# Kernel tuning notes

Measured on AMD Instinct MI355X. Metric: run time of the kernel, lower is better.

## Reference

```python
import jax, jax.numpy as jnp
import numpy as np

B, C, N = 8, 256, 1024
D, DK, DV, H, NB = 256, 16, 32, 8, 4
P = N + 1


def layernorm(x, g, b, eps=1e-5):
    m = x.mean(-1, keepdims=True)
    v = x.var(-1, keepdims=True)
    return (x - m) / jnp.sqrt(v + eps) * g + b


def bn_inf(x, g, b, mean, var, eps=1e-5):
    # x: [B, C', N]; stats over channel dim
    scale = (g / jnp.sqrt(var + eps))[None, :, None]
    shift = (b - mean * g / jnp.sqrt(var + eps))[None, :, None]
    return x * scale + shift


def softmax_with_policy(attn, policy, eps=1e-6):
    # attn: [B,H,P,P], policy: [B,P,1]
    n = attn.shape[-1]
    ap = policy.reshape(policy.shape[0], 1, 1, n)
    eye = jnp.eye(n, dtype=ap.dtype)[None, None]
    ap = ap + (1.0 - ap) * eye
    m = attn.max(-1, keepdims=True)
    e = jnp.exp(attn - m) * ap
    return (e + eps / n) / (e.sum(-1, keepdims=True) + eps)


def setup_inputs() -> dict:
    key = jax.random.key(0)
    ks = jax.random.split(key, 24)
    s = 0.02
    inp = {
        'x': jax.random.normal(ks[0], (B, C, N), jnp.float32),
        'policy': jnp.ones((B, P, 1), jnp.float32),
        'conv1_w': jax.random.normal(ks[1], (D, C), jnp.float32) * s,
        'conv2_w': jax.random.normal(ks[2], (D, D), jnp.float32) * s,
        'bn1_g': jnp.ones((D,), jnp.float32),
        'bn1_b': jnp.zeros((D,), jnp.float32),
        'bn1_m': jax.random.normal(ks[3], (D,), jnp.float32) * s,
        'bn1_v': jax.random.uniform(ks[4], (D,), jnp.float32, 0.5, 1.5),
        'bn2_g': jnp.ones((D,), jnp.float32),
        'bn2_b': jnp.zeros((D,), jnp.float32),
        'bn2_m': jax.random.normal(ks[5], (D,), jnp.float32) * s,
        'bn2_v': jax.random.uniform(ks[6], (D,), jnp.float32, 0.5, 1.5),
        'cls_token': jax.random.normal(ks[7], (D,), jnp.float32),
        'ln1_g': jnp.ones((NB, D), jnp.float32),
        'ln1_b': jnp.zeros((NB, D), jnp.float32),
        'ln2_g': jnp.ones((NB, D), jnp.float32),
        'ln2_b': jnp.zeros((NB, D), jnp.float32),
        'wq': jax.random.normal(ks[8], (NB, H * DK, D), jnp.float32) * np.sqrt(2.0 / (D + DK)).astype(np.float32),
        'wk': jax.random.normal(ks[9], (NB, H * DK, D), jnp.float32) * np.sqrt(2.0 / (D + DK)).astype(np.float32),
        'wv': jax.random.normal(ks[10], (NB, H * DV, D), jnp.float32) * np.sqrt(2.0 / (D + DV)).astype(np.float32),
        'fc_w': jax.random.normal(ks[11], (NB, D, H * DV), jnp.float32) * s,
        'ff_w1': jax.random.normal(ks[12], (NB, 2 * D, D), jnp.float32) * s,
        'ff_b1': jnp.zeros((NB, 2 * D), jnp.float32),
        'ff_w2': jax.random.normal(ks[13], (NB, D, 2 * D), jnp.float32) * s,
        'ff_b2': jnp.zeros((NB, D), jnp.float32),
    }
    return inp


def reference(x, policy, conv1_w, conv2_w, bn1_g, bn1_b, bn1_m, bn1_v,
              bn2_g, bn2_b, bn2_m, bn2_v, cls_token,
              ln1_g, ln1_b, ln2_g, ln2_b, wq, wk, wv, fc_w,
              ff_w1, ff_b1, ff_w2, ff_b2):
    # stem: 1x1 conv + BN(inference) + ReLU, twice. x: [B, C, N]
    h = jax.nn.relu(bn_inf(jnp.einsum('dc,bcn->bdn', conv1_w, x), bn1_g, bn1_b, bn1_m, bn1_v))
    h = jax.nn.relu(bn_inf(jnp.einsum('dc,bcn->bdn', conv2_w, h), bn2_g, bn2_b, bn2_m, bn2_v))
    h = h.transpose(0, 2, 1)  # [B, N, D]
    cls = jnp.broadcast_to(cls_token[None, None, :], (B, 1, D))
    h = jnp.concatenate([cls, h], axis=1)  # [B, P, D]

    scale = 1.0 / np.sqrt(DK).astype(np.float32)
    for i in range(NB):
        # attention
        y = layernorm(h, ln1_g[i], ln1_b[i])
        q = jnp.einsum('bnd,ed->bne', y, wq[i]).reshape(B, P, H, DK).transpose(0, 2, 1, 3)
        k = jnp.einsum('bnd,ed->bne', y, wk[i]).reshape(B, P, H, DK).transpose(0, 2, 1, 3)
        v = jnp.einsum('bnd,ed->bne', y, wv[i]).reshape(B, P, H, DV).transpose(0, 2, 1, 3)
        attn = jnp.einsum('bhlk,bhtk->bhlt', q, k) * scale
        attn = softmax_with_policy(attn, policy)
        o = jnp.einsum('bhlt,bhtv->bhlv', attn, v)  # [B,H,P,DV]
        o = o.transpose(0, 2, 1, 3).reshape(B, P, H * DV)
        h = h + jnp.einsum('bne,de->bnd', o, fc_w[i])
        # feed-forward
        y = layernorm(h, ln2_g[i], ln2_b[i])
        y = jax.nn.gelu(jnp.einsum('bnd,ed->bne', y, ff_w1[i]) + ff_b1[i], approximate=False)
        h = h + jnp.einsum('bne,de->bnd', y, ff_w2[i]) + ff_b2[i]
    return h
```

## Files before the change

kernel.cpp:

```cpp
#include <hip/hip_runtime.h>
#include <stdint.h>


typedef unsigned short u16;
typedef unsigned int   u32;
typedef __bf16 bf16x8 __attribute__((ext_vector_type(8)));
typedef float  f32x4  __attribute__((ext_vector_type(4)));
typedef float  f32x16 __attribute__((ext_vector_type(16)));
typedef u32    u32x4  __attribute__((ext_vector_type(4)));

#define DEV static __device__ __forceinline__

DEV float b2f(u16 h){ u32 u = ((u32)h) << 16; return __builtin_bit_cast(float, u); }
DEV u16 f2b(float f){ u32 u = __builtin_bit_cast(u32, f); u32 r = (u + 0x7fffu + ((u >> 16) & 1u)) >> 16; return (u16)r; }
DEV float gelu_f(float x){ return 0.5f * x * (1.0f + erff(x * 0.7071067811865475f)); }
DEV u32 cvtpk(float lo, float hi){
  u32 w;
  asm("v_cvt_pk_bf16_f32 %0, %1, %2" : "=v"(w) : "v"(lo), "v"(hi));
  return w;
}
DEV float exp2_(float x){ float r; asm("v_exp_f32 %0, %1" : "=v"(r) : "v"(x)); return r; }

typedef void __attribute__((address_space(1)))* gas_t;
typedef void __attribute__((address_space(3)))* las_t;
DEV void cp16(const void* g, void* l){
  __builtin_amdgcn_global_load_lds((gas_t)(uintptr_t)g, (las_t)(uintptr_t)l, 16, 0, 0);
}

struct Seg { const float* src; u16* dst; int n; int period; int dstride; int block0; float scale; };
struct SegPack { Seg s[8]; };

__global__ __launch_bounds__(256) void k_convert(SegPack p){
  int bid = blockIdx.x;
  int si = 0;
  #pragma unroll
  for (int i = 1; i < 8; i++) if (bid >= p.s[i].block0) si = i;
  const Seg sg = p.s[si];
  int e0 = (bid - sg.block0) * 2048 + threadIdx.x * 8;
  #pragma unroll
  for (int k = 0; k < 8; k++){
    int e = e0 + k;
    if (e < sg.n) sg.dst[(e / sg.period) * sg.dstride + (e % sg.period)] = f2b(sg.src[e] * sg.scale);
  }
}

__global__ __launch_bounds__(256) void k_transpose_x(const float* __restrict__ x, u16* __restrict__ xT){
  __shared__ float t[32][33];
  int b = blockIdx.z, ct = blockIdx.y, nt = blockIdx.x;
  int tx = threadIdx.x & 31, ty = threadIdx.x >> 5;
  const float* xp = x + ((size_t)b * 256 + ct * 32) * 1024 + nt * 32;
  #pragma unroll
  for (int k = 0; k < 4; k++) t[ty + 8*k][tx] = xp[(size_t)(ty + 8*k) * 1024 + tx];
  __syncthreads();
  u16* op = xT + ((size_t)b * 1024 + nt * 32) * 256 + ct * 32;
  #pragma unroll
  for (int k = 0; k < 4; k++) op[(size_t)(ty + 8*k) * 256 + tx] = f2b(t[tx][ty + 8*k]);
}

__global__ void k_cls(const float* __restrict__ cls, float* __restrict__ h){
  int d = threadIdx.x;
  #pragma unroll
  for (int b = 0; b < 8; b++) h[(size_t)b * 1025 * 256 + d] = cls[d];
}

__global__ __launch_bounds__(256) void k_ln(const float* __restrict__ h, const float* __restrict__ g,
                                            const float* __restrict__ bt, u16* __restrict__ y){
  int lane = threadIdx.x & 63, wv = threadIdx.x >> 6;
  long t = (long)blockIdx.x * 4 + wv;
  if (t >= 8200) return;
  const float* row = h + t * 256;
  float4 v = *reinterpret_cast<const float4*>(row + lane * 4);
  float s = v.x + v.y + v.z + v.w;
  float q = v.x*v.x + v.y*v.y + v.z*v.z + v.w*v.w;
  #pragma unroll
  for (int o = 32; o > 0; o >>= 1){ s += __shfl_xor(s, o); q += __shfl_xor(q, o); }
  float mean = s * (1.f/256.f);
  float var  = q * (1.f/256.f) - mean * mean;
  float rs = rsqrtf(var + 1e-5f);
  ushort4 ov;
  const float* vp = &v.x;
  u16* o16 = (u16*)&ov;
  #pragma unroll
  for (int j = 0; j < 4; j++){
    int c = lane * 4 + j;
    o16[j] = f2b((vp[j] - mean) * rs * g[c] + bt[c]);
  }
  *reinterpret_cast<ushort4*>(y + t * 256 + lane * 4) = ov;
}

template<int EPI, int BM, int BN>
__global__ __launch_bounds__(256) void k_gemmT(const u16* __restrict__ A, const u16* __restrict__ W,
    int M, int K, int E, float* __restrict__ outF, u16* __restrict__ outB,
    u16* __restrict__ outK,
    const float* __restrict__ a0, const float* __restrict__ a1,
    const float* __restrict__ a2, const float* __restrict__ a3){
  constexpr int MR = BM / 32, NR = BN / 32;
  __shared__ __align__(16) u16 As[BM * 64];
  __shared__ __align__(16) u16 Bs[BN * 64];
  const int tid = threadIdx.x;
  const int lane = tid & 63, wv = tid >> 6;
  const int wr = wv >> 1, wc = wv & 1;
  const int tM = blockIdx.x * BM, tN = blockIdx.y * BN;
  f32x4 acc[MR][NR];
  #pragma unroll
  for (int m = 0; m < MR; m++)
    #pragma unroll
    for (int n = 0; n < NR; n++)
      #pragma unroll
      for (int j = 0; j < 4; j++) acc[m][n][j] = 0.f;

  const int l8 = lane >> 3, lm = lane & 7;
  for (int k0 = 0; k0 < K; k0 += 64){
    __syncthreads();
    #pragma unroll
    for (int is = 0; is < BM / 32; is++){
      int row = is * 32 + wv * 8 + l8;
      int kg = lm ^ (row & 7);
      int ra = tM + row; ra = ra < M ? ra : M - 1;
      cp16(A + (size_t)ra * K + k0 + kg * 8, As + is * 2048 + wv * 512);
    }
    #pragma unroll
    for (int is = 0; is < BN / 32; is++){
      int row = is * 32 + wv * 8 + l8;
      int kg = lm ^ (row & 7);
      cp16(W + (size_t)(tN + row) * K + k0 + kg * 8, Bs + is * 2048 + wv * 512);
    }
    __syncthreads();
    #pragma unroll
    for (int kk = 0; kk < 2; kk++){
      bf16x8 af[MR], bfv[NR];
      #pragma unroll
      for (int m = 0; m < MR; m++){
        int row = wr * (BM/2) + m * 16 + (lane & 15);
        int kg = (kk * 4 + (lane >> 4)) ^ (row & 7);
        af[m] = *reinterpret_cast<const bf16x8*>(&As[row * 64 + kg * 8]);
      }
      #pragma unroll
      for (int n = 0; n < NR; n++){
        int row = wc * (BN/2) + n * 16 + (lane & 15);
        int kg = (kk * 4 + (lane >> 4)) ^ (row & 7);
        bfv[n] = *reinterpret_cast<const bf16x8*>(&Bs[row * 64 + kg * 8]);
      }
      #pragma unroll
      for (int m = 0; m < MR; m++)
        #pragma unroll
        for (int n = 0; n < NR; n++)
          acc[m][n] = __builtin_amdgcn_mfma_f32_16x16x32_bf16(af[m], bfv[n], acc[m][n], 0, 0, 0);
    }
  }
  #pragma unroll
  for (int n = 0; n < NR; n++){
    const int col = tN + wc * (BN/2) + n * 16 + (lane & 15);
    float scale = 0.f, shift = 0.f, bias = 0.f;
    if (EPI == 1 || EPI == 2){
      float gv = a0[col], bv = a1[col], mv = a2[col], vv = a3[col];
      scale = gv * rsqrtf(vv + 1e-5f);
      shift = bv - mv * scale;
    }
    if (EPI == 4 || EPI == 5) bias = a0[col];
    #pragma unroll
    for (int m = 0; m < MR; m++){
      const int row0 = tM + wr * (BM/2) + m * 16 + ((lane >> 4) << 2);
      #pragma unroll
      for (int j = 0; j < 4; j++){
        int r = row0 + j;
        if (r < M){
          float v = acc[m][n][j];
          if (EPI == 1){ v = v * scale + shift; v = v > 0.f ? v : 0.f; outB[(size_t)r * E + col] = f2b(v); }
          else if (EPI == 2){ v = v * scale + shift; v = v > 0.f ? v : 0.f; outF[(size_t)(r + (r >> 10) + 1) * 256 + col] = v; }
          else if (EPI == 3){ outF[(size_t)r * E + col] += v; }
          else if (EPI == 4){ outB[(size_t)r * E + col] = f2b(gelu_f(v + bias)); }
          else if (EPI == 5){ outF[(size_t)r * E + col] += v + bias; }
          else {
            int bb = r / 1025, tok = r - bb * 1025;
            if (col < 128){
              outB[(size_t)r * 512 + col] = f2b(v);
            } else if (col < 256){
              int hk = (col - 128) >> 4, dk = col & 15;
              outK[((size_t)((bb * 8 + hk) * 1032 + tok)) * 16 + dk] = f2b(v);
            } else {
              u16 bv = f2b(v);
              outB[(size_t)r * 512 + col] = bv;
              u16* vt = (u16*)outF;
              int hv = (col - 256) >> 5, dv = (col - 256) & 31;
              vt[((size_t)((bb * 8 + hv) * 32 + dv)) * 1032 + tok] = bv;
            }
          }
        }
      }
    }
  }
}

__global__ __launch_bounds__(256) void k_attn(const u16* __restrict__ qkv,
    const u16* __restrict__ kb, const u16* __restrict__ vt,
    const float* __restrict__ pol, u16* __restrict__ o){
  __shared__ float pol_s[1088];
  __shared__ float oB[3][32][33];
  __shared__ float lsB[3][32];
  const int tid = threadIdx.x;
  const int lane = tid & 63, wv = tid >> 6;
  const int l32 = lane & 31, hi = lane >> 5;
  const int bid = blockIdx.x;
  const int xcd = bid & 7, idx = bid >> 3;
  const int bh = xcd * 8 + idx / 33, qt = idx % 33;
  const int b = bh >> 3, hh = bh & 7;
  const size_t rowbase = (size_t)b * 1025;
  const u16* kbh = kb + (size_t)bh * 1032 * 16;
  const int qg = qt * 32 + l32;
  const int qr = qg > 1024 ? 1024 : qg;
  const bf16x8 qf = *reinterpret_cast<const bf16x8*>(qkv + (rowbase + qr) * 512 + hh * 16 + hi * 8);
  float sqq = 0.f;
  {
    const bf16x8 kown = *reinterpret_cast<const bf16x8*>(kbh + (size_t)qr * 16 + hi * 8);
    #pragma unroll
    for (int i = 0; i < 8; i++) sqq += (float)qf[i] * (float)kown[i];
    sqq += __shfl_xor(sqq, 32);
  }
  const u16* vrow = vt + ((size_t)(bh * 32 + l32)) * 1032;
  for (int t = tid; t < 1088; t += 256){
    float p = (t <= 1024) ? pol[rowbase + t] : 0.f;
    pol_s[t] = (p > 0.f) ? __log2f(p) : -1.0e30f;
  }
  __syncthreads();

  float ls = 0.f;
  f32x16 oacc;
  #pragma unroll
  for (int r = 0; r < 16; r++) oacc[r] = 0.f;

  const int nt = (wv == 0) ? 5 : 4;
  for (int it = 0; it < nt; it++){
    const int jt = (it < 4) ? (wv * 4 + it) : 16;
    const int jb = jt * 64;
    #pragma unroll
    for (int sub = 0; sub < 2; sub++){
      const int jb32 = jb + sub * 32;
      int jrow = jb32 + l32; if (jrow > 1024) jrow = 1024;
      const bf16x8 ka = *reinterpret_cast<const bf16x8*>(kbh + (size_t)jrow * 16 + hi * 8);
      f32x16 fz;
      #pragma unroll
      for (int r = 0; r < 16; r++) fz[r] = 0.f;
      f32x16 st = __builtin_amdgcn_mfma_f32_32x32x16_bf16(ka, qf, fz, 0, 0, 0);
      float e[16];
      float psum = 0.f;
      #pragma unroll
      for (int r = 0; r < 16; r++){
        int jg2 = jb32 + (r & 3) + 8 * (r >> 2) + 4 * hi;
        float ev = exp2_(st[r] + pol_s[jg2]);
        e[r] = ev;
        psum += ev;
      }
      psum += __shfl_xor(psum, 32);
      ls += psum;
      #pragma unroll
      for (int c = 0; c < 2; c++){
        u32 A0 = cvtpk(e[c*8+0], e[c*8+1]);
        u32 A1 = cvtpk(e[c*8+2], e[c*8+3]);
        u32 B0 = cvtpk(e[c*8+4], e[c*8+5]);
        u32 B1 = cvtpk(e[c*8+6], e[c*8+7]);
        u32 pA0 = __shfl_xor(A0, 32), pB0 = __shfl_xor(B0, 32);
        u32 pA1 = __shfl_xor(A1, 32), pB1 = __shfl_xor(B1, 32);
        u32x4 pw;
        pw.x = hi ? pB0 : A0;
        pw.y = hi ? pB1 : A1;
        pw.z = hi ? B0 : pA0;
        pw.w = hi ? B1 : pA1;
        bf16x8 pb = __builtin_bit_cast(bf16x8, pw);
        bf16x8 va = *reinterpret_cast<const bf16x8*>(vrow + jb32 + c * 16 + hi * 8);
        oacc = __builtin_amdgcn_mfma_f32_32x32x16_bf16(va, pb, oacc, 0, 0, 0);
      }
    }
  }
  __syncthreads();
  if (wv > 0){
    lsB[wv-1][l32] = ls;
    #pragma unroll
    for (int r = 0; r < 16; r++) oB[wv-1][l32][(r & 3) + 8 * (r >> 2) + 4 * hi] = oacc[r];
  }
  __syncthreads();
  if (wv == 0 && qg <= 1024){
    float ls_t = ls + lsB[0][l32] + lsB[1][l32] + lsB[2][l32];
    const float pq = exp2_(pol_s[qg]);
    const float ec = (1.f - pq) * exp2_(sqq);
    ls_t += ec;
    const float inv = 1.f / (ls_t + 1e-6f);
    u16* orow = o + (rowbase + qg) * 256 + hh * 32;
    const u16* vq = qkv + (rowbase + qg) * 512 + 256 + hh * 32;
    #pragma unroll
    for (int rq = 0; rq < 4; rq++){
      const int dv0 = 8 * rq + 4 * hi;
      const ushort4 vv4 = *reinterpret_cast<const ushort4*>(vq + dv0);
      const u16* vv = (const u16*)&vv4;
      uint2 wout;
      u32* wp = &wout.x;
      #pragma unroll
      for (int j2 = 0; j2 < 2; j2++){
        const int d0 = dv0 + j2 * 2;
        float v0 = (oacc[rq*4 + j2*2    ] + oB[0][l32][d0    ] + oB[1][l32][d0    ] + oB[2][l32][d0    ] + ec * b2f(vv[j2*2    ])) * inv;
        float v1 = (oacc[rq*4 + j2*2 + 1] + oB[0][l32][d0 + 1] + oB[1][l32][d0 + 1] + oB[2][l32][d0 + 1] + ec * b2f(vv[j2*2 + 1])) * inv;
        wp[j2] = ((u32)f2b(v1) << 16) | (u32)f2b(v0);
      }
      *reinterpret_cast<uint2*>(orow + dv0) = wout;
    }
  }
}

extern "C" void kernel_launch(void* const* d_in, const int* in_sizes, int n_in,
                              void* d_out, int out_size, void* d_ws, size_t ws_size,
                              hipStream_t stream){
  const float* x    = (const float*)d_in[0];
  const float* pol  = (const float*)d_in[1];
  const float* c1w  = (const float*)d_in[2];
  const float* c2w  = (const float*)d_in[3];
  const float* bn1g = (const float*)d_in[4];
  const float* bn1b = (const float*)d_in[5];
  const float* bn1m = (const float*)d_in[6];
  const float* bn1v = (const float*)d_in[7];
  const float* bn2g = (const float*)d_in[8];
  const float* bn2b = (const float*)d_in[9];
  const float* bn2m = (const float*)d_in[10];
  const float* bn2v = (const float*)d_in[11];
  const float* cls  = (const float*)d_in[12];
  const float* ln1g = (const float*)d_in[13];
  const float* ln1b = (const float*)d_in[14];
  const float* ln2g = (const float*)d_in[15];
  const float* ln2b = (const float*)d_in[16];
  const float* wq   = (const float*)d_in[17];
  const float* wk   = (const float*)d_in[18];
  const float* wvp  = (const float*)d_in[19];
  const float* fcw  = (const float*)d_in[20];
  const float* ffw1 = (const float*)d_in[21];
  const float* ffb1 = (const float*)d_in[22];
  const float* ffw2 = (const float*)d_in[23];
  const float* ffb2 = (const float*)d_in[24];
  float* h = (float*)d_out;

  u16* ws   = (u16*)d_ws;
  u16* wc1  = ws;
  u16* wc2  = wc1  + 65536;
  u16* wqkv = wc2  + 65536;
  u16* wfc  = wqkv + 524288;
  u16* wff1 = wfc  + 262144;
  u16* wff2 = wff1 + 524288;
  u16* xT   = wff2 + 524288;
  u16* h1   = xT   + 2097152;
  u16* yb   = h1   + 2097152;
  u16* qkvb = yb   + 2099200;
  u16* ob   = qkvb + 4198400;
  u16* vtb  = ob   + 2099200;
  u16* kbb  = vtb  + 2117632;
  u16* ub   = qkvb;

  const float QSCALE = 0.25f * 1.4426950408889634f;
  SegPack sp;
  int b0 = 0;
  sp.s[0] = Seg{ c1w,  wc1,          65536,  65536,  0,      b0, 1.f }; b0 += 32;
  sp.s[1] = Seg{ c2w,  wc2,          65536,  65536,  0,      b0, 1.f }; b0 += 32;
  sp.s[2] = Seg{ wq,   wqkv,         131072, 32768,  131072, b0, QSCALE }; b0 += 64;
  sp.s[3] = Seg{ wk,   wqkv + 32768, 131072, 32768,  131072, b0, 1.f }; b0 += 64;
  sp.s[4] = Seg{ wvp,  wqkv + 65536, 262144, 65536,  131072, b0, 1.f }; b0 += 128;
  sp.s[5] = Seg{ fcw,  wfc,          262144, 262144, 0,      b0, 1.f }; b0 += 128;
  sp.s[6] = Seg{ ffw1, wff1,         524288, 524288, 0,      b0, 1.f }; b0 += 256;
  sp.s[7] = Seg{ ffw2, wff2,         524288, 524288, 0,      b0, 1.f }; b0 += 256;

  k_convert<<<b0, 256, 0, stream>>>(sp);
  k_transpose_x<<<dim3(32, 8, 8), 256, 0, stream>>>(x, xT);
  k_cls<<<1, 256, 0, stream>>>(cls, h);
  k_gemmT<1,64,64><<<dim3(128, 4), 256, 0, stream>>>(xT, wc1, 8192, 256, 256, nullptr, h1, nullptr,
                                                     bn1g, bn1b, bn1m, bn1v);
  k_gemmT<2,64,64><<<dim3(128, 4), 256, 0, stream>>>(h1, wc2, 8192, 256, 256, h, nullptr, nullptr,
                                                     bn2g, bn2b, bn2m, bn2v);
  for (int i = 0; i < 4; i++){
    k_ln<<<2050, 256, 0, stream>>>(h, ln1g + i*256, ln1b + i*256, yb);
    k_gemmT<6,64,128><<<dim3(129, 4), 256, 0, stream>>>(yb, wqkv + i*131072, 8200, 256, 512,
                                                        (float*)vtb, qkvb, kbb,
                                                        nullptr, nullptr, nullptr, nullptr);
    k_attn<<<2112, 256, 0, stream>>>(qkvb, kbb, vtb, pol, ob);
    k_gemmT<3,64,64><<<dim3(129, 4), 256, 0, stream>>>(ob, wfc + i*65536, 8200, 256, 256, h, nullptr, nullptr,
                                                       nullptr, nullptr, nullptr, nullptr);
    k_ln<<<2050, 256, 0, stream>>>(h, ln2g + i*256, ln2b + i*256, yb);
    k_gemmT<4,64,128><<<dim3(129, 4), 256, 0, stream>>>(yb, wff1 + i*131072, 8200, 256, 512, nullptr, ub, nullptr,
                                                        ffb1 + i*512, nullptr, nullptr, nullptr);
    k_gemmT<5,64,64><<<dim3(129, 4), 256, 0, stream>>>(ub, wff2 + i*131072, 8200, 512, 256, h, nullptr, nullptr,
                                                       ffb2 + i*256, nullptr, nullptr, nullptr);
  }
}
```

Before: 384.1 us.

## Add single-shot K=256 GEMM kernel and special-case CLS key in attention

Introduces k_g256, which loads the full K=256 slab of A and W into shared memory at once (64x64 tile, 64KB LDS) and then runs eight MFMA k-steps with no further syncs. It replaces the tiled k-loop GEMMs for conv1, conv2, QKV, fc and ff1; QKV and ff1 now use 64x64 tiles and twice as many blocks. Separately, attention drops the extra fifth key tile that wave 0 used to process for the CLS token and instead adds the CLS key/value contribution analytically in the epilogue. The larger LDS footprint may limit occupancy, and the single load phase gives no overlap of memory with compute.

```diff
diff --git a/kernel.cpp b/kernel.cpp
--- a/kernel.cpp
+++ b/kernel.cpp
@@ -88,79 +88,74 @@
   *reinterpret_cast<ushort4*>(y + t * 256 + lane * 4) = ov;
 }
 
-template<int EPI, int BM, int BN>
-__global__ __launch_bounds__(256) void k_gemmT(const u16* __restrict__ A, const u16* __restrict__ W,
-    int M, int K, int E, float* __restrict__ outF, u16* __restrict__ outB,
-    u16* __restrict__ outK,
+template<int EPI>
+__global__ __launch_bounds__(256) void k_g256(const u16* __restrict__ A, const u16* __restrict__ W,
+    int M, int E, float* __restrict__ outF, u16* __restrict__ outB, u16* __restrict__ outK,
     const float* __restrict__ a0, const float* __restrict__ a1,
     const float* __restrict__ a2, const float* __restrict__ a3){
-  constexpr int MR = BM / 32, NR = BN / 32;
-  __shared__ __align__(16) u16 As[BM * 64];
-  __shared__ __align__(16) u16 Bs[BN * 64];
+  __shared__ __align__(16) u16 As[64 * 256];
+  __shared__ __align__(16) u16 Bs[64 * 256];
   const int tid = threadIdx.x;
   const int lane = tid & 63, wv = tid >> 6;
   const int wr = wv >> 1, wc = wv & 1;
-  const int tM = blockIdx.x * BM, tN = blockIdx.y * BN;
-  f32x4 acc[MR][NR];
-  #pragma unroll
-  for (int m = 0; m < MR; m++)
-    #pragma unroll
-    for (int n = 0; n < NR; n++)
+  const int tM = blockIdx.x * 64, tN = blockIdx.y * 64;
+
+  #pragma unroll
+  for (int ii = 0; ii < 8; ii++){
+    const int i = wv * 8 + ii;
+    const int row = 2 * i + (lane >> 5);
+    const int gS = (lane & 31) ^ (row & 7);
+    int ra = tM + row; ra = ra < M ? ra : M - 1;
+    cp16(A + (size_t)ra * 256 + gS * 8, As + i * 512);
+    cp16(W + (size_t)(tN + row) * 256 + gS * 8, Bs + i * 512);
+  }
+  __syncthreads();
+
+  f32x4 acc[2][2];
+  #pragma unroll
+  for (int m = 0; m < 2; m++)
+    #pragma unroll
+    for (int n = 0; n < 2; n++)
       #pragma unroll
       for (int j = 0; j < 4; j++) acc[m][n][j] = 0.f;
 
-  const int l8 = lane >> 3, lm = lane & 7;
-  for (int k0 = 0; k0 < K; k0 += 64){
-    __syncthreads();
-    #pragma unroll
-    for (int is = 0; is < BM / 32; is++){
-      int row = is * 32 + wv * 8 + l8;
-      int kg = lm ^ (row & 7);
-      int ra = tM + row; ra = ra < M ? ra : M - 1;
-      cp16(A + (size_t)ra * K + k0 + kg * 8, As + is * 2048 + wv * 512);
-    }
-    #pragma unroll
-    for (int is = 0; is < BN / 32; is++){
-      int row = is * 32 + wv * 8 + l8;
-      int kg = lm ^ (row & 7);
-      cp16(W + (size_t)(tN + row) * K + k0 + kg * 8, Bs + is * 2048 + wv * 512);
-    }
-    __syncthreads();
-    #pragma unroll
-    for (int kk = 0; kk < 2; kk++){
-      bf16x8 af[MR], bfv[NR];
-      #pragma unroll
-      for (int m = 0; m < MR; m++){
-        int row = wr * (BM/2) + m * 16 + (lane & 15);
-        int kg = (kk * 4 + (lane >> 4)) ^ (row & 7);
-        af[m] = *reinterpret_cast<const bf16x8*>(&As[row * 64 + kg * 8]);
-      }
-      #pragma unroll
-      for (int n = 0; n < NR; n++){
-        int row = wc * (BN/2) + n * 16 + (lane & 15);
-        int kg = (kk * 4 + (lane >> 4)) ^ (row & 7);
-        bfv[n] = *reinterpret_cast<const bf16x8*>(&Bs[row * 64 + kg * 8]);
-      }
-      #pragma unroll
-      for (int m = 0; m < MR; m++)
-        #pragma unroll
-        for (int n = 0; n < NR; n++)
-          acc[m][n] = __builtin_amdgcn_mfma_f32_16x16x32_bf16(af[m], bfv[n], acc[m][n], 0, 0, 0);
-    }
-  }
-  #pragma unroll
-  for (int n = 0; n < NR; n++){
-    const int col = tN + wc * (BN/2) + n * 16 + (lane & 15);
+  const int rA0 = wr * 32 + (lane & 15);
+  const int rB0 = wc * 32 + (lane & 15);
+  #pragma unroll
+  for (int t = 0; t < 8; t++){
+    bf16x8 af[2], bfv[2];
+    #pragma unroll
+    for (int m = 0; m < 2; m++){
+      const int row = rA0 + m * 16;
+      const int g = (t * 4 + (lane >> 4)) ^ (row & 7);
+      af[m] = *reinterpret_cast<const bf16x8*>(&As[row * 256 + g * 8]);
+    }
+    #pragma unroll
+    for (int n = 0; n < 2; n++){
+      const int row = rB0 + n * 16;
+      const int g = (t * 4 + (lane >> 4)) ^ (row & 7);
+      bfv[n] = *reinterpret_cast<const bf16x8*>(&Bs[row * 256 + g * 8]);
+    }
+    #pragma unroll
+    for (int m = 0; m < 2; m++)
+      #pragma unroll
+      for (int n = 0; n < 2; n++)
+        acc[m][n] = __builtin_amdgcn_mfma_f32_16x16x32_bf16(af[m], bfv[n], acc[m][n], 0, 0, 0);
+  }
+
+  #pragma unroll
+  for (int n = 0; n < 2; n++){
+    const int col = tN + wc * 32 + n * 16 + (lane & 15);
     float scale = 0.f, shift = 0.f, bias = 0.f;
     if (EPI == 1 || EPI == 2){
       float gv = a0[col], bv = a1[col], mv = a2[col], vv = a3[col];
       scale = gv * rsqrtf(vv + 1e-5f);
       shift = bv - mv * scale;
     }
-    if (EPI == 4 || EPI == 5) bias = a0[col];
-    #pragma unroll
-    for (int m = 0; m < MR; m++){
-      const int row0 = tM + wr * (BM/2) + m * 16 + ((lane >> 4) << 2);
+    if (EPI == 4) bias = a0[col];
+    #pragma unroll
+    for (int m = 0; m < 2; m++){
+      const int row0 = tM + wr * 32 + m * 16 + ((lane >> 4) << 2);
       #pragma unroll
       for (int j = 0; j < 4; j++){
         int r = row0 + j;
@@ -170,7 +165,6 @@
           else if (EPI == 2){ v = v * scale + shift; v = v > 0.f ? v : 0.f; outF[(size_t)(r + (r >> 10) + 1) * 256 + col] = v; }
           else if (EPI == 3){ outF[(size_t)r * E + col] += v; }
           else if (EPI == 4){ outB[(size_t)r * E + col] = f2b(gelu_f(v + bias)); }
-          else if (EPI == 5){ outF[(size_t)r * E + col] += v + bias; }
           else {
             int bb = r / 1025, tok = r - bb * 1025;
             if (col < 128){
@@ -186,6 +180,84 @@
               vt[((size_t)((bb * 8 + hv) * 32 + dv)) * 1032 + tok] = bv;
             }
           }
+        }
+      }
+    }
+  }
+}
+
+template<int EPI, int BM, int BN>
+__global__ __launch_bounds__(256) void k_gemmT(const u16* __restrict__ A, const u16* __restrict__ W,
+    int M, int K, int E, float* __restrict__ outF, u16* __restrict__ outB,
+    const float* __restrict__ a0){
+  constexpr int MR = BM / 32, NR = BN / 32;
+  __shared__ __align__(16) u16 As[BM * 64];
+  __shared__ __align__(16) u16 Bs[BN * 64];
+  const int tid = threadIdx.x;
+  const int lane = tid & 63, wv = tid >> 6;
+  const int wr = wv >> 1, wc = wv & 1;
+  const int tM = blockIdx.x * BM, tN = blockIdx.y * BN;
+  f32x4 acc[MR][NR];
+  #pragma unroll
+  for (int m = 0; m < MR; m++)
+    #pragma unroll
+    for (int n = 0; n < NR; n++)
+      #pragma unroll
+      for (int j = 0; j < 4; j++) acc[m][n][j] = 0.f;
+
+  const int l8 = lane >> 3, lm = lane & 7;
+  for (int k0 = 0; k0 < K; k0 += 64){
+    __syncthreads();
+    #pragma unroll
+    for (int is = 0; is < BM / 32; is++){
+      int row = is * 32 + wv * 8 + l8;
+      int kg = lm ^ (row & 7);
+      int ra = tM + row; ra = ra < M ? ra : M - 1;
+      cp16(A + (size_t)ra * K + k0 + kg * 8, As + is * 2048 + wv * 512);
+    }
+    #pragma unroll
+    for (int is = 0; is < BN / 32; is++){
+      int row = is * 32 + wv * 8 + l8;
+      int kg = lm ^ (row & 7);
+      cp16(W + (size_t)(tN + row) * K + k0 + kg * 8, Bs + is * 2048 + wv * 512);
+    }
+    __syncthreads();
+    #pragma unroll
+    for (int kk = 0; kk < 2; kk++){
+      bf16x8 af[MR], bfv[NR];
+      #pragma unroll
+      for (int m = 0; m < MR; m++){
+        int row = wr * (BM/2) + m * 16 + (lane & 15);
+        int kg = (kk * 4 + (lane >> 4)) ^ (row & 7);
+        af[m] = *reinterpret_cast<const bf16x8*>(&As[row * 64 + kg * 8]);
+      }
+      #pragma unroll
+      for (int n = 0; n < NR; n++){
+        int row = wc * (BN/2) + n * 16 + (lane & 15);
+        int kg = (kk * 4 + (lane >> 4)) ^ (row & 7);
+        bfv[n] = *reinterpret_cast<const bf16x8*>(&Bs[row * 64 + kg * 8]);
+      }
+      #pragma unroll
+      for (int m = 0; m < MR; m++)
+        #pragma unroll
+        for (int n = 0; n < NR; n++)
+          acc[m][n] = __builtin_amdgcn_mfma_f32_16x16x32_bf16(af[m], bfv[n], acc[m][n], 0, 0, 0);
+    }
+  }
+  #pragma unroll
+  for (int n = 0; n < NR; n++){
+    const int col = tN + wc * (BN/2) + n * 16 + (lane & 15);
+    float bias = (EPI == 5) ? a0[col] : 0.f;
+    #pragma unroll
+    for (int m = 0; m < MR; m++){
+      const int row0 = tM + wr * (BM/2) + m * 16 + ((lane >> 4) << 2);
+      #pragma unroll
+      for (int j = 0; j < 4; j++){
+        int r = row0 + j;
+        if (r < M){
+          float v = acc[m][n][j];
+          if (EPI == 3){ outF[(size_t)r * E + col] += v; }
+          else { outF[(size_t)r * E + col] += v + bias; }
         }
       }
     }
@@ -210,12 +282,17 @@
   const int qg = qt * 32 + l32;
   const int qr = qg > 1024 ? 1024 : qg;
   const bf16x8 qf = *reinterpret_cast<const bf16x8*>(qkv + (rowbase + qr) * 512 + hh * 16 + hi * 8);
-  float sqq = 0.f;
+  float sqq = 0.f, scl = 0.f;
   {
     const bf16x8 kown = *reinterpret_cast<const bf16x8*>(kbh + (size_t)qr * 16 + hi * 8);
-    #pragma unroll
-    for (int i = 0; i < 8; i++) sqq += (float)qf[i] * (float)kown[i];
+    const bf16x8 kcls = *reinterpret_cast<const bf16x8*>(kbh + (size_t)1024 * 16 + hi * 8);
+    #pragma unroll
+    for (int i = 0; i < 8; i++){
+      sqq += (float)qf[i] * (float)kown[i];
+      scl += (float)qf[i] * (float)kcls[i];
+    }
     sqq += __shfl_xor(sqq, 32);
+    scl += __shfl_xor(scl, 32);
   }
   const u16* vrow = vt + ((size_t)(bh * 32 + l32)) * 1032;
   for (int t = tid; t < 1088; t += 256){
@@ -229,15 +306,13 @@
   #pragma unroll
   for (int r = 0; r < 16; r++) oacc[r] = 0.f;
 
-  const int nt = (wv == 0) ? 5 : 4;
-  for (int it = 0; it < nt; it++){
-    const int jt = (it < 4) ? (wv * 4 + it) : 16;
-    const int jb = jt * 64;
+  #pragma unroll
+  for (int it = 0; it < 4; it++){
+    const int jb = (wv * 4 + it) * 64;
     #pragma unroll
     for (int sub = 0; sub < 2; sub++){
       const int jb32 = jb + sub * 32;
-      int jrow = jb32 + l32; if (jrow > 1024) jrow = 1024;
-      const bf16x8 ka = *reinterpret_cast<const bf16x8*>(kbh + (size_t)jrow * 16 + hi * 8);
+      const bf16x8 ka = *reinterpret_cast<const bf16x8*>(kbh + (size_t)(jb32 + l32) * 16 + hi * 8);
       f32x16 fz;
       #pragma unroll
       for (int r = 0; r < 16; r++) fz[r] = 0.f;
@@ -283,22 +358,28 @@
     float ls_t = ls + lsB[0][l32] + lsB[1][l32] + lsB[2][l32];
     const float pq = exp2_(pol_s[qg]);
     const float ec = (1.f - pq) * exp2_(sqq);
-    ls_t += ec;
+    const float ecl = exp2_(scl + pol_s[1024]);
+    ls_t += ec + ecl;
     const float inv = 1.f / (ls_t + 1e-6f);
     u16* orow = o + (rowbase + qg) * 256 + hh * 32;
-    const u16* vq = qkv + (rowbase + qg) * 512 + 256 + hh * 32;
+    const u16* vq   = qkv + (rowbase + qg) * 512 + 256 + hh * 32;
+    const u16* vcls = qkv + (rowbase + 1024) * 512 + 256 + hh * 32;
     #pragma unroll
     for (int rq = 0; rq < 4; rq++){
       const int dv0 = 8 * rq + 4 * hi;
       const ushort4 vv4 = *reinterpret_cast<const ushort4*>(vq + dv0);
+      const ushort4 vc4 = *reinterpret_cast<const ushort4*>(vcls + dv0);
       const u16* vv = (const u16*)&vv4;
+      const u16* vc = (const u16*)&vc4;
       uint2 wout;
       u32* wp = &wout.x;
       #pragma unroll
       for (int j2 = 0; j2 < 2; j2++){
         const int d0 = dv0 + j2 * 2;
-        float v0 = (oacc[rq*4 + j2*2    ] + oB[0][l32][d0    ] + oB[1][l32][d0    ] + oB[2][l32][d0    ] + ec * b2f(vv[j2*2    ])) * inv;
-        float v1 = (oacc[rq*4 + j2*2 + 1] + oB[0][l32][d0 + 1] + oB[1][l32][d0 + 1] + oB[2][l32][d0 + 1] + ec * b2f(vv[j2*2 + 1])) * inv;
+        float v0 = (oacc[rq*4 + j2*2    ] + oB[0][l32][d0    ] + oB[1][l32][d0    ] + oB[2][l32][d0    ]
+                    + ec * b2f(vv[j2*2    ]) + ecl * b2f(vc[j2*2    ])) * inv;
+        float v1 = (oacc[rq*4 + j2*2 + 1] + oB[0][l32][d0 + 1] + oB[1][l32][d0 + 1] + oB[2][l32][d0 + 1]
+                    + ec * b2f(vv[j2*2 + 1]) + ecl * b2f(vc[j2*2 + 1])) * inv;
         wp[j2] = ((u32)f2b(v1) << 16) | (u32)f2b(v0);
       }
       *reinterpret_cast<uint2*>(orow + dv0) = wout;
@@ -367,22 +448,22 @@
   k_convert<<<b0, 256, 0, stream>>>(sp);
   k_transpose_x<<<dim3(32, 8, 8), 256, 0, stream>>>(x, xT);
   k_cls<<<1, 256, 0, stream>>>(cls, h);
-  k_gemmT<1,64,64><<<dim3(128, 4), 256, 0, stream>>>(xT, wc1, 8192, 256, 256, nullptr, h1, nullptr,
-                                                     bn1g, bn1b, bn1m, bn1v);
-  k_gemmT<2,64,64><<<dim3(128, 4), 256, 0, stream>>>(h1, wc2, 8192, 256, 256, h, nullptr, nullptr,
-                                                     bn2g, bn2b, bn2m, bn2v);
+  k_g256<1><<<dim3(128, 4), 256, 0, stream>>>(xT, wc1, 8192, 256, nullptr, h1, nullptr,
+                                              bn1g, bn1b, bn1m, bn1v);
+  k_g256<2><<<dim3(128, 4), 256, 0, stream>>>(h1, wc2, 8192, 256, h, nullptr, nullptr,
+                                              bn2g, bn2b, bn2m, bn2v);
   for (int i = 0; i < 4; i++){
     k_ln<<<2050, 256, 0, stream>>>(h, ln1g + i*256, ln1b + i*256, yb);
-    k_gemmT<6,64,128><<<dim3(129, 4), 256, 0, stream>>>(yb, wqkv + i*131072, 8200, 256, 512,
-                                                        (float*)vtb, qkvb, kbb,
-                                                        nullptr, nullptr, nullptr, nullptr);
+    k_g256<6><<<dim3(129, 8), 256, 0, stream>>>(yb, wqkv + i*131072, 8200, 512,
+                                                (float*)vtb, qkvb, kbb,
+                                                nullptr, nullptr, nullptr, nullptr);
     k_attn<<<2112, 256, 0, stream>>>(qkvb, kbb, vtb, pol, ob);
-    k_gemmT<3,64,64><<<dim3(129, 4), 256, 0, stream>>>(ob, wfc + i*65536, 8200, 256, 256, h, nullptr, nullptr,
-                                                       nullptr, nullptr, nullptr, nullptr);
+    k_g256<3><<<dim3(129, 4), 256, 0, stream>>>(ob, wfc + i*65536, 8200, 256, h, nullptr, nullptr,
+                                                nullptr, nullptr, nullptr, nullptr);
     k_ln<<<2050, 256, 0, stream>>>(h, ln2g + i*256, ln2b + i*256, yb);
-    k_gemmT<4,64,128><<<dim3(129, 4), 256, 0, stream>>>(yb, wff1 + i*131072, 8200, 256, 512, nullptr, ub, nullptr,
-                                                        ffb1 + i*512, nullptr, nullptr, nullptr);
-    k_gemmT<5,64,64><<<dim3(129, 4), 256, 0, stream>>>(ub, wff2 + i*131072, 8200, 512, 256, h, nullptr, nullptr,
-                                                       ffb2 + i*256, nullptr, nullptr, nullptr);
-  }
-}
+    k_g256<4><<<dim3(129, 8), 256, 0, stream>>>(yb, wff1 + i*131072, 8200, 512, nullptr, ub, nullptr,
+                                                ffb1 + i*512, nullptr, nullptr, nullptr);
+    k_gemmT<5,64,64><<<dim3(129, 4), 256, 0, stream>>>(ub, wff2 + i*131072, 8200, 512, 256, h, nullptr,
+                                                       ffb2 + i*256);
+  }
+}
```

Result: slower. 412.5 us (+7.4%).
